# Kernel optimization log

Measured on AMD Instinct MI355X. Metric: run time of the kernel, lower is better.

## Reference

```python
import jax, jax.numpy as jnp
import numpy as np

N_SEGMENT = 8
N_DIV = 8


def _shift_weights(cq, n_div):
    fold = cq // n_div
    w1 = np.zeros((cq, 1, 1, 1, 1), np.float32); w1[:, 0, 0] = 1.0
    w3 = np.zeros((cq, 1, 3, 1, 1), np.float32)
    w3[:fold, 0, 0] = 1.0; w3[fold:2 * fold, 0, 2] = 1.0; w3[2 * fold:, 0, 1] = 1.0
    w5 = np.zeros((cq, 1, 5, 1, 1), np.float32)
    w5[:fold, 0, :2] = 1.0; w5[fold:2 * fold, 0, 3:] = 1.0; w5[2 * fold:, 0, 2] = 1.0
    w7 = np.zeros((cq, 1, 7, 1, 1), np.float32)
    w7[:fold, 0, :3] = 1.0; w7[fold:2 * fold, 0, 4:] = 1.0; w7[2 * fold:, 0, 3] = 1.0
    return w1, w3, w5, w7


def setup_inputs() -> dict:
    key = jax.random.key(0)
    ks = jax.random.split(key, 5)
    nt, c, h, w = 64, 256, 56, 56
    cq = c // 4  # 64
    x = jax.random.normal(ks[0], (nt, c, h, w), jnp.float32)
    w1, w3, w5, w7 = _shift_weights(cq, N_DIV)
    mk = lambda k: jax.random.normal(k, (cq, cq, 3, 3), jnp.float32) * 0.05
    return {
        'x': x,
        'w1': jnp.asarray(w1), 'w3': jnp.asarray(w3),
        'w5': jnp.asarray(w5), 'w7': jnp.asarray(w7),
        'w21': mk(ks[1]), 'w22': mk(ks[2]), 'w23': mk(ks[3]), 'w24': mk(ks[4]),
    }


def _dwconv_t(x, w, pad):
    # x: (B, Cq, T, H, W); w: (Cq, 1, K, 1, 1); depthwise temporal conv3d
    return jax.lax.conv_general_dilated(
        x, w, window_strides=(1, 1, 1),
        padding=((pad, pad), (0, 0), (0, 0)),
        dimension_numbers=('NCDHW', 'OIDHW', 'NCDHW'),
        feature_group_count=x.shape[1])


def _conv2d(x, w, stride):
    return jax.lax.conv_general_dilated(
        x, w, (stride, stride), ((1, 1), (1, 1)),
        dimension_numbers=('NCHW', 'OIHW', 'NCHW'))


def reference(x, w1, w3, w5, w7, w21, w22, w23, w24):
    nt, c, h, w = x.shape
    cq = c // 4
    b = nt // N_SEGMENT
    # (nt, c, h, w) -> (b, c, T, h, w)
    xt = x.reshape(b, N_SEGMENT, c, h, w).transpose(0, 2, 1, 3, 4)
    parts = [xt[:, i * cq:(i + 1) * cq] for i in range(4)]
    kws = [(w1, 0), (w3, 1), (w5, 2), (w7, 3)]
    outs = []
    for xp, (wk, pad) in zip(parts, kws):
        y = _dwconv_t(xp, wk, pad)  # (b, cq, T, h, w)
        y = y.transpose(0, 2, 1, 3, 4).reshape(nt, cq, h, w)
        outs.append(y)
    stride = 1
    y1 = _conv2d(outs[0], w21, stride)
    y2 = _conv2d(outs[1], w22, stride)
    y3 = _conv2d(outs[2], w23, stride)
    y4 = _conv2d(outs[3], w24, stride)
    return jnp.concatenate((y1, y2, y3, y4), axis=1)
```

## Files before the change

### kernel.cpp

```cpp
#include <hip/hip_runtime.h>

#define HW 3136
#define TSTR (256 * 3136)

typedef __attribute__((ext_vector_type(8))) short bf16x8;
typedef __attribute__((ext_vector_type(4))) float f32x4;

__device__ __forceinline__ short f2bf(float f) {
    union { float f; unsigned u; } c; c.f = f;
    unsigned u = c.u + 0x7fffu + ((c.u >> 16) & 1u);
    return (short)(u >> 16);
}

__global__ void wprep_kernel(const float* __restrict__ w21, const float* __restrict__ w22,
                             const float* __restrict__ w23, const float* __restrict__ w24,
                             short* __restrict__ wt) {
    int i = blockIdx.x * 256 + threadIdx.x;
    if (i >= 4 * 9 * 64 * 64) return;
    int ci = i & 63, co = (i >> 6) & 63, pt = i >> 12;
    int tap = pt % 9, p = pt / 9;
    const float* w2 = p == 0 ? w21 : p == 1 ? w22 : p == 2 ? w23 : w24;
    wt[i] = f2bf(w2[co * 576 + ci * 9 + tap]);
}

__global__ __launch_bounds__(256, 2)
void msg_mfma_kernel(const float* __restrict__ x, const short* __restrict__ wt,
                     float* __restrict__ out) {
    const int rb = blockIdx.x;
    const int p  = blockIdx.y;
    const int n  = blockIdx.z;
    const int y0 = rb * 4;
    const int bi = n >> 3, t = n & 7;

    __shared__ __align__(16) short in_lds[6 * 58 * 40];
    __shared__ __align__(16) short w_lds[9 * 64 * 40];

    const int tid  = threadIdx.x;
    const int lane = tid & 63, wv = tid >> 6;
    const int wr = wv >> 1;
    const int wc = wv & 1;
    const int lm = lane & 15, ciq = lane >> 4;

    int abase[7];
#pragma unroll
    for (int mt = 0; mt < 7; ++mt) {
        int sl = (wr * 7 + mt) * 16 + lm;
        int ry = sl / 56, cx = sl - ry * 56;
        abase[mt] = (ry * 58 + cx) * 40 + ciq * 8;
    }
    int bbase[2];
#pragma unroll
    for (int nt = 0; nt < 2; ++nt)
        bbase[nt] = (wc * 32 + nt * 16 + lm) * 40 + ciq * 8;

    f32x4 acc[7][2];
#pragma unroll
    for (int mt = 0; mt < 7; ++mt)
#pragma unroll
        for (int nt = 0; nt < 2; ++nt)
            acc[mt][nt] = (f32x4){0.f, 0.f, 0.f, 0.f};

    const float* xseg = x + (size_t)bi * 8 * TSTR;
    const short* wt_p = wt + p * (9 * 64 * 64);

    for (int cb = 0; cb < 64; cb += 32) {
        if (cb) __syncthreads();

        for (int e = tid; e < 2880; e += 256) {
            int ci = e & 31;
            int q  = (e >> 5) % 15;
            int ry = (e >> 5) / 15;
            if (q == 14) {
                in_lds[(ry * 58 + 0) * 40 + ci]  = 0;
                in_lds[(ry * 58 + 57) * 40 + ci] = 0;
            } else {
                int cig = cb + ci;
                int gy  = y0 - 1 + ry;
                float vx = 0.f, vy = 0.f, vz = 0.f, vw = 0.f;
                if ((unsigned)gy < 56u) {
                    const float* xb = xseg + (size_t)(p * 64 + cig) * HW + gy * 56 + q * 4;
                    if (p == 0 || cig >= 16) {
                        float4 a = *(const float4*)(xb + (size_t)t * TSTR);
                        vx = a.x; vy = a.y; vz = a.z; vw = a.w;
                    } else if (cig < 8) {
                        for (int d = 1; d <= p; ++d)
                            if (t - d >= 0) {
                                float4 a = *(const float4*)(xb + (size_t)(t - d) * TSTR);
                                vx += a.x; vy += a.y; vz += a.z; vw += a.w;
                            }
                    } else {
                        for (int d = 1; d <= p; ++d)
                            if (t + d < 8) {
                                float4 a = *(const float4*)(xb + (size_t)(t + d) * TSTR);
                                vx += a.x; vy += a.y; vz += a.z; vw += a.w;
                            }
                    }
                }
                int base = (ry * 58 + q * 4 + 1) * 40 + ci;
                in_lds[base]       = f2bf(vx);
                in_lds[base + 40]  = f2bf(vy);
                in_lds[base + 80]  = f2bf(vz);
                in_lds[base + 120] = f2bf(vw);
            }
        }

        for (int e = tid; e < 2304; e += 256) {
            int row = e >> 2, ci8 = (e & 3) << 3;
            *(bf16x8*)&w_lds[row * 40 + ci8] =
                *(const bf16x8*)&wt_p[(row << 6) + cb + ci8];
        }
        __syncthreads();

#pragma unroll
        for (int tap = 0; tap < 9; ++tap) {
            const int ky = tap / 3, kx = tap % 3;
            bf16x8 b0 = *(const bf16x8*)&w_lds[bbase[0] + tap * 2560];
            bf16x8 b1 = *(const bf16x8*)&w_lds[bbase[1] + tap * 2560];
#pragma unroll
            for (int mt = 0; mt < 7; ++mt) {
                bf16x8 a = *(const bf16x8*)&in_lds[abase[mt] + (ky * 58 + kx) * 40];
                acc[mt][0] = __builtin_amdgcn_mfma_f32_16x16x32_bf16(b0, a, acc[mt][0], 0, 0, 0);
                acc[mt][1] = __builtin_amdgcn_mfma_f32_16x16x32_bf16(b1, a, acc[mt][1], 0, 0, 0);
            }
        }
    }

    const size_t obase = ((size_t)n * 256 + p * 64) * HW + (size_t)y0 * 56;
#pragma unroll
    for (int mt = 0; mt < 7; ++mt) {
        int sg = (wr * 7 + mt) * 16 + lm;
#pragma unroll
        for (int nt = 0; nt < 2; ++nt) {
            int co = wc * 32 + nt * 16 + ciq * 4;
#pragma unroll
            for (int j = 0; j < 4; ++j)
                out[obase + (size_t)(co + j) * HW + sg] = acc[mt][nt][j];
        }
    }
}

extern "C" void kernel_launch(void* const* d_in, const int* in_sizes, int n_in,
                              void* d_out, int out_size, void* d_ws, size_t ws_size,
                              hipStream_t stream) {
    const float* x   = (const float*)d_in[0];
    const float* w21 = (const float*)d_in[5];
    const float* w22 = (const float*)d_in[6];
    const float* w23 = (const float*)d_in[7];
    const float* w24 = (const float*)d_in[8];
    short* wt = (short*)d_ws;

    hipLaunchKernelGGL(wprep_kernel, dim3(576), dim3(256), 0, stream,
                       w21, w22, w23, w24, wt);
    hipLaunchKernelGGL(msg_mfma_kernel, dim3(14, 4, 64), dim3(256), 0, stream,
                       x, wt, (float*)d_out);
}
```

Measured before the change: 544.5 us.

## Pre-swizzle weights into MFMA fragment order and load directly from global

The weight-prep kernel now writes bf16 weights in the exact per-lane MFMA B-fragment order, so the main kernel reads each fragment with one coalesced 16-byte global load instead of staging weights through LDS. Removing the weight LDS buffer reduces shared memory per block, and the launch bound is raised to allow 4 blocks per CU for higher occupancy. The cost is global/L2 weight loads sitting on the MFMA inner loop's critical path, and tighter register limits that may cause spills given the 56 accumulator registers.

```diff
diff --git a/kernel.cpp b/kernel.cpp
--- a/kernel.cpp
+++ b/kernel.cpp
@@ -14,16 +14,24 @@
 
 __global__ void wprep_kernel(const float* __restrict__ w21, const float* __restrict__ w22,
                              const float* __restrict__ w23, const float* __restrict__ w24,
-                             short* __restrict__ wt) {
+                             short* __restrict__ wt2) {
     int i = blockIdx.x * 256 + threadIdx.x;
-    if (i >= 4 * 9 * 64 * 64) return;
-    int ci = i & 63, co = (i >> 6) & 63, pt = i >> 12;
-    int tap = pt % 9, p = pt / 9;
+    if (i >= 147456) return;
+    int e    = i & 7;
+    int l    = (i >> 3) & 63;
+    int nt   = (i >> 9) & 1;
+    int wc   = (i >> 10) & 1;
+    int tap  = (i >> 11) % 9;
+    int rest = (i >> 11) / 9;
+    int cb2  = rest & 1;
+    int p    = rest >> 1;
     const float* w2 = p == 0 ? w21 : p == 1 ? w22 : p == 2 ? w23 : w24;
-    wt[i] = f2bf(w2[co * 576 + ci * 9 + tap]);
+    int co = wc * 32 + nt * 16 + (l & 15);
+    int ci = cb2 * 32 + ((l >> 4) << 3) + e;
+    wt2[i] = f2bf(w2[co * 576 + ci * 9 + tap]);
 }
 
-__global__ __launch_bounds__(256, 2)
+__global__ __launch_bounds__(256, 4)
 void msg_mfma_kernel(const float* __restrict__ x, const short* __restrict__ wt,
                      float* __restrict__ out) {
     const int rb = blockIdx.x;
@@ -33,7 +41,6 @@
     const int bi = n >> 3, t = n & 7;
 
     __shared__ __align__(16) short in_lds[6 * 58 * 40];
-    __shared__ __align__(16) short w_lds[9 * 64 * 40];
 
     const int tid  = threadIdx.x;
     const int lane = tid & 63, wv = tid >> 6;
@@ -48,10 +55,6 @@
         int ry = sl / 56, cx = sl - ry * 56;
         abase[mt] = (ry * 58 + cx) * 40 + ciq * 8;
     }
-    int bbase[2];
-#pragma unroll
-    for (int nt = 0; nt < 2; ++nt)
-        bbase[nt] = (wc * 32 + nt * 16 + lm) * 40 + ciq * 8;
 
     f32x4 acc[7][2];
 #pragma unroll
@@ -61,10 +64,12 @@
             acc[mt][nt] = (f32x4){0.f, 0.f, 0.f, 0.f};
 
     const float* xseg = x + (size_t)bi * 8 * TSTR;
-    const short* wt_p = wt + p * (9 * 64 * 64);
+    const bf16x8* wt2p = (const bf16x8*)wt + p * 4608;
 
-    for (int cb = 0; cb < 64; cb += 32) {
-        if (cb) __syncthreads();
+#pragma unroll
+    for (int cb2 = 0; cb2 < 2; ++cb2) {
+        const int cb = cb2 * 32;
+        if (cb2) __syncthreads();
 
         for (int e = tid; e < 2880; e += 256) {
             int ci = e & 31;
@@ -103,19 +108,14 @@
                 in_lds[base + 120] = f2bf(vw);
             }
         }
-
-        for (int e = tid; e < 2304; e += 256) {
-            int row = e >> 2, ci8 = (e & 3) << 3;
-            *(bf16x8*)&w_lds[row * 40 + ci8] =
-                *(const bf16x8*)&wt_p[(row << 6) + cb + ci8];
-        }
         __syncthreads();
 
 #pragma unroll
         for (int tap = 0; tap < 9; ++tap) {
             const int ky = tap / 3, kx = tap % 3;
-            bf16x8 b0 = *(const bf16x8*)&w_lds[bbase[0] + tap * 2560];
-            bf16x8 b1 = *(const bf16x8*)&w_lds[bbase[1] + tap * 2560];
+            const int fi = (cb2 * 9 + tap) * 4 + wc * 2;
+            bf16x8 b0 = wt2p[(fi + 0) * 64 + lane];
+            bf16x8 b1 = wt2p[(fi + 1) * 64 + lane];
 #pragma unroll
             for (int mt = 0; mt < 7; ++mt) {
                 bf16x8 a = *(const bf16x8*)&in_lds[abase[mt] + (ky * 58 + kx) * 40];
@@ -147,10 +147,10 @@
     const float* w22 = (const float*)d_in[6];
     const float* w23 = (const float*)d_in[7];
     const float* w24 = (const float*)d_in[8];
-    short* wt = (short*)d_ws;
+    short* wt2 = (short*)d_ws;
 
     hipLaunchKernelGGL(wprep_kernel, dim3(576), dim3(256), 0, stream,
-                       w21, w22, w23, w24, wt);
+                       w21, w22, w23, w24, wt2);
     hipLaunchKernelGGL(msg_mfma_kernel, dim3(14, 4, 64), dim3(256), 0, stream,
-                       x, wt, (float*)d_out);
+                       x, wt2, (float*)d_out);
 }
```

Measured after the change: 508.4 us. -6.6%, faster.
